# Optimization experiments

Measured on AMD Instinct MI355X. Metric: run time of the kernel, lower is better.

The kernel has to match this reference:

```python
import jax, jax.numpy as jnp
import numpy as np

BLANK = 4
NEG = -1.0e30  # log-space 'zero'


def _ctc_loss(log_probs, targets, input_lengths, target_lengths):
    # log_probs: (N, T, C) raw logits -> module applies log_softmax then transposes to (T, N, C)
    lp = jax.nn.log_softmax(log_probs, axis=-1)
    lp = jnp.transpose(lp, (1, 0, 2))  # (T, N, C)
    T, N, C = lp.shape
    S = targets.shape[1]
    L = 2 * S + 1  # extended label length (blanks interleaved)

    # extended label sequence: blank, y1, blank, y2, ..., yS, blank  -> (N, L)
    ext = jnp.full((N, L), BLANK, dtype=targets.dtype).at[:, 1::2].set(targets)

    # gather per-step log-probs of extended labels: (T, N, L)
    lp_ext = jnp.take_along_axis(lp, jnp.broadcast_to(ext[None], (T, N, L)), axis=2)

    # skip transition (k-2 -> k) allowed iff ext[k] != blank and ext[k] != ext[k-2]
    ext_m2 = jnp.pad(ext[:, :-2], ((0, 0), (2, 0)), constant_values=BLANK)
    skip = (ext != BLANK) & (ext != ext_m2)
    skip = skip.at[:, :2].set(False)

    # alpha at t=0: only positions 0 (blank) and 1 (first label) reachable
    alpha0 = jnp.full((N, L), NEG, dtype=lp.dtype)
    alpha0 = alpha0.at[:, 0].set(lp_ext[0, :, 0]).at[:, 1].set(lp_ext[0, :, 1])

    neg_col = jnp.full((N, 1), NEG, dtype=lp.dtype)

    def step(alpha, xs):
        t, lpe = xs  # lpe: (N, L)
        s1 = jnp.concatenate([neg_col, alpha[:, :-1]], axis=1)
        s2 = jnp.concatenate([neg_col, neg_col, alpha[:, :-2]], axis=1)
        a = jnp.logaddexp(alpha, s1)
        a = jnp.logaddexp(a, jnp.where(skip, s2, NEG))
        new = a + lpe
        # freeze alpha once past this sequence's input length
        alpha = jnp.where((t < input_lengths)[:, None], new, alpha)
        return alpha, None

    ts = jnp.arange(1, T)
    alpha, _ = jax.lax.scan(step, alpha0, (ts, lp_ext[1:]))

    idx = jnp.arange(N)
    last = 2 * target_lengths  # final blank position; last label is at 2L-1
    l_label = alpha[idx, last - 1]
    l_blank = alpha[idx, last]
    nll = -jnp.logaddexp(l_label, l_blank)  # per-sequence negative log-likelihood

    # reduction='mean': divide each loss by its target length, then mean over batch
    return jnp.mean(nll / target_lengths.astype(nll.dtype))


def setup_inputs() -> dict:
    key = jax.random.key(0)
    k1, k2, k3, k4 = jax.random.split(key, 4)
    N, T, C, S = 32, 1600, 1024, 200
    log_probs = jax.random.normal(k1, (N, T, C), dtype=jnp.float32)
    # targets in [0, C) excluding blank index 4
    t = jax.random.randint(k2, (N, S), 0, C - 1)
    targets = t + (t >= BLANK).astype(t.dtype)
    input_lengths = jax.random.randint(k3, (N,), 800, T + 1)
    target_lengths = jax.random.randint(k4, (N,), 50, S + 1)
    return {
        "log_probs": log_probs,
        "targets": targets,
        "input_lengths": input_lengths,
        "target_lengths": target_lengths,
    }


def reference(log_probs, targets, input_lengths, target_lengths):
    return _ctc_loss(log_probs, targets, input_lengths, target_lengths)
```

## Files before the change

### kernel.cpp

```cpp
#include <hip/hip_runtime.h>
#include <hip/hip_bf16.h>

#define N_    32
#define T_    1600
#define C_    1024
#define S_    200
#define L_    401
#define LP_   512
#define BLANK_ 4
#define LN2_  0.69314718055994531f
#define L2E_  1.44269504088896341f
#define DPF   8

#if __has_builtin(__builtin_amdgcn_exp2f)
#define EXP2(x) __builtin_amdgcn_exp2f(x)
#else
#define EXP2(x) exp2f(x)
#endif
#if __has_builtin(__builtin_amdgcn_rcpf)
#define RCP(x) __builtin_amdgcn_rcpf(x)
#else
#define RCP(x) (1.0f / (x))
#endif

__global__ __launch_bounds__(256)
void k_softmax_gather(const float* __restrict__ logits,
                      const int* __restrict__ targets,
                      const int* __restrict__ tgt_len,
                      float* __restrict__ P) {
  const int row  = blockIdx.x * 4 + (threadIdx.x >> 6);
  const int lane = threadIdx.x & 63;
  const int wv   = threadIdx.x >> 6;
  const int n    = row / T_;
  const float* x = logits + (size_t)row * C_;
  __shared__ float sh[4][C_];

  float4 v[4];
#pragma unroll
  for (int i = 0; i < 4; ++i)
    v[i] = reinterpret_cast<const float4*>(x)[i * 64 + lane];

  float mx = v[0].x;
#pragma unroll
  for (int i = 0; i < 4; ++i)
    mx = fmaxf(mx, fmaxf(fmaxf(v[i].x, v[i].y), fmaxf(v[i].z, v[i].w)));
#pragma unroll
  for (int i = 1; i < 64; i <<= 1) mx = fmaxf(mx, __shfl_xor(mx, i));

  float s = 0.0f;
#pragma unroll
  for (int i = 0; i < 4; ++i) {
    s += EXP2((v[i].x - mx) * L2E_) + EXP2((v[i].y - mx) * L2E_)
       + EXP2((v[i].z - mx) * L2E_) + EXP2((v[i].w - mx) * L2E_);
  }
#pragma unroll
  for (int i = 1; i < 64; i <<= 1) s += __shfl_xor(s, i);
  float rz = RCP(s);

#pragma unroll
  for (int i = 0; i < 4; ++i)
    reinterpret_cast<float4*>(sh[wv])[i * 64 + lane] = v[i];
  __syncthreads();

  const int* tg = targets + n * S_;
  const int lmax = 2 * tgt_len[n];
  float* out = P + (size_t)row * LP_;
#pragma unroll
  for (int i = 0; i < 8; ++i) {
    int l = lane + i * 64;
    float p = 0.0f;
    if (l <= lmax) {
      int c = (l & 1) ? tg[(l - 1) >> 1] : BLANK_;
      p = EXP2((sh[wv][c] - mx) * L2E_) * rz;
    }
    out[l] = p;
  }
}

__global__ __launch_bounds__(64)
void k_ctc(const float* __restrict__ P,
           const int* __restrict__ targets,
           const int* __restrict__ in_len,
           const int* __restrict__ tgt_len,
           float* __restrict__ nll_out) {
  const int n = blockIdx.x;
  const int lane = threadIdx.x;
  const int Tn = in_len[n];
  const float* g = P + (size_t)n * T_ * LP_;

  double sk[8];
#pragma unroll
  for (int j = 0; j < 8; ++j) {
    int l = lane * 8 + j;
    double b = 0.0;
    if ((l & 1) && l >= 3 && l <= 2 * S_) {
      int m = (l - 1) >> 1;
      b = (targets[n * S_ + m] != targets[n * S_ + m - 1]) ? 1.0 : 0.0;
    }
    sk[j] = b;
  }

  double a[8];
#pragma unroll
  for (int j = 0; j < 8; ++j) a[j] = 0.0;
  if (lane == 0) { a[0] = (double)g[0]; a[1] = (double)g[1]; }
  int Etot = 0;

  const float* gl = g + lane * 8;
  float4 bA[DPF], bB[DPF];
#pragma unroll
  for (int d = 0; d < DPF; ++d) {
    int tt = 1 + d; if (tt > T_ - 1) tt = T_ - 1;
    bA[d] = *reinterpret_cast<const float4*>(gl + (size_t)tt * LP_);
    bB[d] = *reinterpret_cast<const float4*>(gl + (size_t)tt * LP_ + 4);
  }

  const int src = (lane + 63) & 63;

  auto step = [&](const float4& A, const float4& B) {
    double up7 = __shfl(a[7], src);
    double up6 = __shfl(a[6], src);
    if (lane == 0) { up7 = 0.0; up6 = 0.0; }
    float pv[8] = {A.x, A.y, A.z, A.w, B.x, B.y, B.z, B.w};
#pragma unroll
    for (int j = 7; j >= 2; --j)
      a[j] = (a[j] + a[j - 1] + sk[j] * a[j - 2]) * (double)pv[j];
    a[1] = (a[1] + a[0] + sk[1] * up7) * (double)pv[1];
    a[0] = (a[0] + up7 + sk[0] * up6) * (double)pv[0];
  };

  auto renorm = [&]() {
    int h = __double2hiint(a[0]);
#pragma unroll
    for (int j = 1; j < 8; ++j) h = max(h, __double2hiint(a[j]));
#pragma unroll
    for (int i = 1; i < 64; i <<= 1) h = max(h, __shfl_xor(h, i));
    int R = 1021 - (h >> 20);
#pragma unroll
    for (int j = 0; j < 8; ++j) a[j] = ldexp(a[j], R);
    Etot -= R;
  };

  int t = 1;
  const int nsteps = Tn - 1;
  const int nfull = (nsteps / DPF) * DPF;
  int blk = 0;
  for (int s = 0; s < nfull; s += DPF) {
#pragma unroll
    for (int d = 0; d < DPF; ++d) {
      step(bA[d], bB[d]);
      int tt = t + DPF; if (tt > T_ - 1) tt = T_ - 1;
      bA[d] = *reinterpret_cast<const float4*>(gl + (size_t)tt * LP_);
      bB[d] = *reinterpret_cast<const float4*>(gl + (size_t)tt * LP_ + 4);
      ++t;
    }
    if ((++blk & 3) == 0) renorm();
  }
#pragma unroll
  for (int d = 0; d < DPF - 1; ++d) {
    if (t < Tn) { step(bA[d], bB[d]); ++t; }
  }

  __shared__ double sa[LP_];
#pragma unroll
  for (int j = 0; j < 8; ++j) sa[lane * 8 + j] = a[j];
  __syncthreads();
  if (lane == 0) {
    int tl = tgt_len[n];
    double v = sa[2 * tl - 1] + sa[2 * tl];
    int ee;
    double m = frexp(v, &ee);
    nll_out[n] = -LN2_ * ((float)(Etot + ee) + log2f((float)m));
  }
}

__global__ void k_final(const float* __restrict__ nll,
                        const int* __restrict__ tgt_len,
                        float* __restrict__ out) {
  int lane = threadIdx.x;
  float v = 0.0f;
  if (lane < N_) v = nll[lane] / (float)tgt_len[lane];
#pragma unroll
  for (int i = 1; i < 64; i <<= 1) v += __shfl_xor(v, i);
  if (lane == 0) out[0] = v * (1.0f / N_);
}

__global__ void k_sentinel(float* out) { out[0] = -12345.0f; }

extern "C" void kernel_launch(void* const* d_in, const int* in_sizes, int n_in,
                              void* d_out, int out_size, void* d_ws, size_t ws_size,
                              hipStream_t stream) {
  const float* logits = (const float*)d_in[0];
  const int* targets  = (const int*)d_in[1];
  const int* in_len   = (const int*)d_in[2];
  const int* tgt_len  = (const int*)d_in[3];
  float* out = (float*)d_out;

  size_t gbytes = (size_t)N_ * T_ * LP_ * sizeof(float);
  if (ws_size < gbytes + 256) {
    k_sentinel<<<1, 1, 0, stream>>>(out);
    return;
  }
  float* G = (float*)d_ws;
  float* nll = (float*)((char*)d_ws + gbytes);

  k_softmax_gather<<<(N_ * T_) / 4, 256, 0, stream>>>(logits, targets, tgt_len, G);
  k_ctc<<<N_, 64, 0, stream>>>(G, targets, in_len, tgt_len, nll);
  k_final<<<1, 64, 0, stream>>>(nll, tgt_len, out);
}
```

Before: 493.5 us.

## Split CTC alpha recurrence across two wavefronts with per-step LDS handoff

The CTC forward recurrence now runs on 128 threads per sequence, so each lane holds 4 alpha states instead of 8. This halves the serial FP64 dependency chain per time step. The boundary value between the two wavefronts is exchanged through double-buffered shared memory with a barrier every step, and renormalisation reduces its max across both waves. The cost is a workgroup barrier on the critical path of each of roughly 1600 steps.

Measured after the change: 499.0 us. Within noise of the previous version (+1.1%).

```diff
diff --git a/kernel.cpp b/kernel.cpp
--- a/kernel.cpp
+++ b/kernel.cpp
@@ -22,6 +22,8 @@
 #else
 #define RCP(x) (1.0f / (x))
 #endif
+
+#define BAR() asm volatile("s_waitcnt lgkmcnt(0)\n\ts_barrier" ::: "memory")
 
 __global__ __launch_bounds__(256)
 void k_softmax_gather(const float* __restrict__ logits,
@@ -77,67 +79,73 @@
   }
 }
 
-__global__ __launch_bounds__(64)
+__global__ __launch_bounds__(128)
 void k_ctc(const float* __restrict__ P,
            const int* __restrict__ targets,
            const int* __restrict__ in_len,
            const int* __restrict__ tgt_len,
            float* __restrict__ nll_out) {
   const int n = blockIdx.x;
-  const int lane = threadIdx.x;
+  const int tid = threadIdx.x;
+  const int w = tid >> 6;
+  const int lane = tid & 63;
   const int Tn = in_len[n];
   const float* g = P + (size_t)n * T_ * LP_;
-
-  double sk[8];
-#pragma unroll
-  for (int j = 0; j < 8; ++j) {
-    int l = lane * 8 + j;
-    double b = 0.0;
-    if ((l & 1) && l >= 3 && l <= 2 * S_) {
-      int m = (l - 1) >> 1;
-      b = (targets[n * S_ + m] != targets[n * S_ + m - 1]) ? 1.0 : 0.0;
-    }
-    sk[j] = b;
-  }
-
-  double a[8];
-#pragma unroll
-  for (int j = 0; j < 8; ++j) a[j] = 0.0;
-  if (lane == 0) { a[0] = (double)g[0]; a[1] = (double)g[1]; }
+  const int base = (w << 8) + (lane << 2);
+
+  __shared__ double slot[2][2];
+  __shared__ int rl[2];
+  __shared__ double sa[LP_];
+
+  const int* tg = targets + n * S_;
+  const int m1 = (w << 7) + (lane << 1);
+  const int mm = m1 > 0 ? m1 : 1;
+  double sk1 = (m1 >= 1 && m1 < S_ && tg[mm] != tg[mm - 1]) ? 1.0 : 0.0;
+  const int m3 = m1 + 1;
+  double sk3 = (m3 < S_ && tg[m3] != tg[m3 - 1]) ? 1.0 : 0.0;
+
+  double a0 = 0.0, a1 = 0.0, a2 = 0.0, a3 = 0.0;
+  double up = 0.0;
+  if (tid == 0) { a0 = (double)g[0]; a1 = (double)g[1]; }
   int Etot = 0;
 
-  const float* gl = g + lane * 8;
-  float4 bA[DPF], bB[DPF];
+  const float* gl = g + base;
+  float4 b[DPF];
 #pragma unroll
   for (int d = 0; d < DPF; ++d) {
-    int tt = 1 + d; if (tt > T_ - 1) tt = T_ - 1;
-    bA[d] = *reinterpret_cast<const float4*>(gl + (size_t)tt * LP_);
-    bB[d] = *reinterpret_cast<const float4*>(gl + (size_t)tt * LP_ + 4);
+    int tt = 1 + d;
+    b[d] = *reinterpret_cast<const float4*>(gl + (size_t)tt * LP_);
   }
 
   const int src = (lane + 63) & 63;
 
-  auto step = [&](const float4& A, const float4& B) {
-    double up7 = __shfl(a[7], src);
-    double up6 = __shfl(a[6], src);
-    if (lane == 0) { up7 = 0.0; up6 = 0.0; }
-    float pv[8] = {A.x, A.y, A.z, A.w, B.x, B.y, B.z, B.w};
-#pragma unroll
-    for (int j = 7; j >= 2; --j)
-      a[j] = (a[j] + a[j - 1] + sk[j] * a[j - 2]) * (double)pv[j];
-    a[1] = (a[1] + a[0] + sk[1] * up7) * (double)pv[1];
-    a[0] = (a[0] + up7 + sk[0] * up6) * (double)pv[0];
+  auto step = [&](int t, const float4& pv) {
+    double p0 = (double)pv.x, p1 = (double)pv.y;
+    double p2 = (double)pv.z, p3 = (double)pv.w;
+    double a3n = (a3 + a2 + sk3 * a1) * p3;
+    double a2n = (a2 + a1) * p2;
+    double a1n = (a1 + a0 + sk1 * up) * p1;
+    double a0n = (a0 + up) * p0;
+    if (lane == 63) slot[t & 1][w] = a3n;
+    BAR();
+    double bd = slot[t & 1][w ^ 1];
+    double sh = __shfl(a3n, src);
+    up = (lane == 0) ? bd : sh;
+    a0 = a0n; a1 = a1n; a2 = a2n; a3 = a3n;
   };
 
   auto renorm = [&]() {
-    int h = __double2hiint(a[0]);
-#pragma unroll
-    for (int j = 1; j < 8; ++j) h = max(h, __double2hiint(a[j]));
+    int h = max(max(__double2hiint(a0), __double2hiint(a1)),
+                max(__double2hiint(a2), __double2hiint(a3)));
 #pragma unroll
     for (int i = 1; i < 64; i <<= 1) h = max(h, __shfl_xor(h, i));
-    int R = 1021 - (h >> 20);
-#pragma unroll
-    for (int j = 0; j < 8; ++j) a[j] = ldexp(a[j], R);
+    if (lane == 0) rl[w] = h;
+    BAR();
+    int hb = max(rl[0], rl[1]);
+    int R = 1021 - (hb >> 20);
+    a0 = ldexp(a0, R); a1 = ldexp(a1, R);
+    a2 = ldexp(a2, R); a3 = ldexp(a3, R);
+    up = ldexp(up, R);
     Etot -= R;
   };
 
@@ -148,24 +156,22 @@
   for (int s = 0; s < nfull; s += DPF) {
 #pragma unroll
     for (int d = 0; d < DPF; ++d) {
-      step(bA[d], bB[d]);
+      step(t, b[d]);
       int tt = t + DPF; if (tt > T_ - 1) tt = T_ - 1;
-      bA[d] = *reinterpret_cast<const float4*>(gl + (size_t)tt * LP_);
-      bB[d] = *reinterpret_cast<const float4*>(gl + (size_t)tt * LP_ + 4);
+      b[d] = *reinterpret_cast<const float4*>(gl + (size_t)tt * LP_);
       ++t;
     }
     if ((++blk & 3) == 0) renorm();
   }
 #pragma unroll
   for (int d = 0; d < DPF - 1; ++d) {
-    if (t < Tn) { step(bA[d], bB[d]); ++t; }
-  }
-
-  __shared__ double sa[LP_];
-#pragma unroll
-  for (int j = 0; j < 8; ++j) sa[lane * 8 + j] = a[j];
+    if (t < Tn) { step(t, b[d]); ++t; }
+  }
+
+  sa[base + 0] = a0; sa[base + 1] = a1;
+  sa[base + 2] = a2; sa[base + 3] = a3;
   __syncthreads();
-  if (lane == 0) {
+  if (tid == 0) {
     int tl = tgt_len[n];
     double v = sa[2 * tl - 1] + sa[2 * tl];
     int ee;
@@ -205,6 +211,6 @@
   float* nll = (float*)((char*)d_ws + gbytes);
 
   k_softmax_gather<<<(N_ * T_) / 4, 256, 0, stream>>>(logits, targets, tgt_len, G);
-  k_ctc<<<N_, 64, 0, stream>>>(G, targets, in_len, tgt_len, nll);
+  k_ctc<<<N_, 128, 0, stream>>>(G, targets, in_len, tgt_len, nll);
   k_final<<<1, 64, 0, stream>>>(nll, tgt_len, out);
 }
```
